# Kernel optimization log

Measured on AMD Instinct MI355X. Metric: run time of the kernel, lower is better.

## Reference

```python
import jax, jax.numpy as jnp
import numpy as np

N = 50000      # nodes
E = 400000     # edges (avg degree 8)
C = 128        # dim_single (node_dim)
DP = 64        # dim_pair (edge_dim)
HID = 256      # dim_egnn_hidden
DEPTH = 4      # depth_equivariant
M_IN = 2 * C + DP  # node_mlp / coord_mlp input dim = 320


def setup_inputs() -> dict:
    key = jax.random.key(0)
    ks = jax.random.split(key, 12)
    def w(k, shape, fan):
        return jax.random.normal(k, shape, jnp.float32) / np.float32(np.sqrt(fan))
    return {
        'single': jax.random.normal(ks[0], (N, C), jnp.float32),
        'pair': jax.random.normal(ks[1], (1,), jnp.float32),  # unused (se3t/ipa disabled)
        'coords': jax.random.normal(ks[2], (N, 3), jnp.float32),
        'edge_index': jax.random.randint(ks[3], (2, E), 0, N, jnp.int32),
        'edge_dist': jax.random.uniform(ks[4], (E,), jnp.float32),
        # stacked per-layer EGNN params (leading DEPTH axis, consumed by lax.scan)
        'We1': w(ks[5], (DEPTH, 1, DP), 1), 'be1': jnp.zeros((DEPTH, DP), jnp.float32),
        'We2': w(ks[6], (DEPTH, DP, DP), DP), 'be2': jnp.zeros((DEPTH, DP), jnp.float32),
        'Wn1': w(ks[7], (DEPTH, M_IN, HID), M_IN), 'bn1': jnp.zeros((DEPTH, HID), jnp.float32),
        'Wn2': w(ks[8], (DEPTH, HID, C), HID), 'bn2': jnp.zeros((DEPTH, C), jnp.float32),
        'Wc1': w(ks[9], (DEPTH, M_IN, HID), M_IN), 'bc1': jnp.zeros((DEPTH, HID), jnp.float32),
        'Wc2': w(ks[10], (DEPTH, HID, 1), HID),  # coord_mlp final layer has no bias
        'gamma': jnp.ones((C,), jnp.float32), 'beta': jnp.zeros((C,), jnp.float32),
    }


def _egnn_stack(h, x, edge_index, edge_dist, params):
    src, dst = edge_index[0], edge_index[1]
    n_nodes = h.shape[0]
    def layer(carry, p):
        h, x = carry
        We1, be1, We2, be2, Wn1, bn1, Wn2, bn2, Wc1, bc1, Wc2 = p
        # edge_mlp(edge_dist)
        ea = jax.nn.silu(edge_dist[:, None] @ We1 + be1) @ We2 + be2        # [E, DP]
        # gather -> concat -> MLP (message)
        mi = jnp.concatenate([h[src], h[dst], ea], axis=-1)                 # [E, 2C+DP]
        m = jax.nn.silu(mi @ Wn1 + bn1) @ Wn2 + bn2                         # [E, C]
        h = h + jax.ops.segment_sum(m, dst, num_segments=n_nodes)          # index_add on dst
        # coordinate update
        cw = jax.nn.silu(mi @ Wc1 + bc1) @ Wc2                              # [E, 1]
        x = x + jax.ops.segment_sum(cw * (x[src] - x[dst]), dst, num_segments=n_nodes)
        return (h, x), None
    (h, x), _ = jax.lax.scan(layer, (h, x), params)
    return h, x


def reference(single, pair, coords, edge_index, edge_dist,
              We1, be1, We2, be2, Wn1, bn1, Wn2, bn2, Wc1, bc1, Wc2,
              gamma, beta):
    h, x = _egnn_stack(single, coords, edge_index, edge_dist,
                       (We1, be1, We2, be2, Wn1, bn1, Wn2, bn2, Wc1, bc1, Wc2))
    # final LayerNorm (eps=1e-5, matching nn.LayerNorm default)
    mu = h.mean(-1, keepdims=True)
    var = ((h - mu) ** 2).mean(-1, keepdims=True)
    out = gamma * (h - mu) * jax.lax.rsqrt(var + 1e-5) + beta
    return out, x
```

## Files before the change

### kernel.cpp

```cpp
#include <hip/hip_runtime.h>
#include <hip/hip_bf16.h>
#include <math.h>

#define NN 50000
#define NE 400000
#define CD 128
#define EPB 64
#define HBINS 50176

typedef __attribute__((ext_vector_type(8))) short bf16x8;
typedef __attribute__((ext_vector_type(4))) float f32x4;

__device__ __forceinline__ float silu_f(float z) {
    return z * __builtin_amdgcn_rcpf(1.f + __expf(-z));
}
__device__ __forceinline__ unsigned short f2bf(float x) {
    unsigned int u = __float_as_uint(x);
    u = (u + 0x7FFFu + ((u >> 16) & 1u)) >> 16;
    return (unsigned short)u;
}
__device__ __forceinline__ float bf2f(unsigned short h) {
    return __uint_as_float(((unsigned int)h) << 16);
}
__device__ __forceinline__ unsigned pk_bf16(float a, float b) {
    union { __hip_bfloat162 h2; unsigned u; } cv;
    cv.h2 = __float22bfloat162_rn(make_float2(a, b));
    return cv.u;
}

__global__ __launch_bounds__(256) void hist_kernel(
        const int* __restrict__ dst, int* __restrict__ hist)
{
    int e = blockIdx.x * 256 + threadIdx.x;
    if (e < NE) atomicAdd(&hist[dst[e]], 1);
}

__global__ __launch_bounds__(256) void scan1_kernel(
        const int* __restrict__ hist, int* __restrict__ offs, int* __restrict__ bsum)
{
    __shared__ int sh[256];
    const int t = threadIdx.x;
    const int i = blockIdx.x * 256 + t;
    int v = hist[i];
    sh[t] = v;
    __syncthreads();
    for (int off = 1; off < 256; off <<= 1) {
        int x = (t >= off) ? sh[t - off] : 0;
        __syncthreads();
        sh[t] += x;
        __syncthreads();
    }
    offs[i] = sh[t] - v;
    if (t == 255) bsum[blockIdx.x] = sh[t];
}

__global__ __launch_bounds__(256) void scan2_kernel(int* __restrict__ bsum)
{
    __shared__ int sh[256];
    const int t = threadIdx.x;
    int v = (t < 196) ? bsum[t] : 0;
    sh[t] = v;
    __syncthreads();
    for (int off = 1; off < 256; off <<= 1) {
        int x = (t >= off) ? sh[t - off] : 0;
        __syncthreads();
        sh[t] += x;
        __syncthreads();
    }
    if (t < 196) bsum[t] = sh[t] - v;
}

__global__ __launch_bounds__(256) void scan3_kernel(
        const int* __restrict__ offs, const int* __restrict__ bsum,
        int* __restrict__ cursor)
{
    const int i = blockIdx.x * 256 + threadIdx.x;
    cursor[i] = offs[i] + bsum[blockIdx.x];
}

__global__ __launch_bounds__(256) void scatter_kernel(
        const int* __restrict__ eidx, const float* __restrict__ edist,
        int* __restrict__ cursor,
        int* __restrict__ ssrc, int* __restrict__ sdst, float* __restrict__ sdist)
{
    int e = blockIdx.x * 256 + threadIdx.x;
    if (e < NE) {
        int d = eidx[NE + e];
        int p = atomicAdd(&cursor[d], 1);
        ssrc[p] = eidx[e];
        sdst[p] = d;
        sdist[p] = edist[e];
    }
}

__global__ __launch_bounds__(64) void wbig_prep(
        const float* __restrict__ We2, const float* __restrict__ Wn1,
        const float* __restrict__ Wc1, unsigned short* __restrict__ wbig)
{
    const int l = blockIdx.y;
    const int ntile = blockIdx.x / 10;
    const int ks = blockIdx.x % 10;
    const int lane = threadIdx.x;
    const int n = ntile * 16 + (lane & 15);
    const int kbase = ks * 32 + (lane >> 4) * 8;
    const float* Wn1l = Wn1 + (size_t)l * 320 * 256;
    const float* Wc1l = Wc1 + (size_t)l * 320 * 256;
    const float* We2l = We2 + (size_t)l * 64 * 64;
    const float* W1 = (n < 256) ? Wn1l : Wc1l;
    const int nn = n & 255;
    unsigned short* outp = wbig + ((((size_t)l * 32 + ntile) * 10 + ks) * 64 + lane) * 8;
    #pragma unroll
    for (int j = 0; j < 8; ++j) {
        int k = kbase + j;
        float val;
        if (k < 256) {
            val = W1[(size_t)k * 256 + nn];
        } else {
            int i = k - 256;
            float acc = 0.f;
            #pragma unroll 8
            for (int jj = 0; jj < 64; ++jj)
                acc += We2l[i * 64 + jj] * W1[(size_t)(256 + jj) * 256 + nn];
            val = acc;
        }
        outp[j] = f2bf(val);
    }
}

__global__ __launch_bounds__(64) void wn2_prep(
        const float* __restrict__ Wn2, unsigned short* __restrict__ wn2s)
{
    const int l = blockIdx.y;
    const int ntile = blockIdx.x / 8;
    const int ks = blockIdx.x % 8;
    const int lane = threadIdx.x;
    const int n = ntile * 16 + (lane & 15);
    const int kbase = ks * 32 + (lane >> 4) * 8;
    const float* Wn2l = Wn2 + (size_t)l * 256 * 128;
    unsigned short* outp = wn2s + ((((size_t)l * 8 + ntile) * 8 + ks) * 64 + lane) * 8;
    #pragma unroll
    for (int j = 0; j < 8; ++j)
        outp[j] = f2bf(Wn2l[(size_t)(kbase + j) * 128 + n]);
}

__global__ __launch_bounds__(512) void cep_prep(
        const float* __restrict__ be2,
        const float* __restrict__ Wn1, const float* __restrict__ Wc1,
        const float* __restrict__ bn1, const float* __restrict__ bc1,
        float* __restrict__ cep)
{
    const int l = blockIdx.x;
    const int j = threadIdx.x;
    const int jj = j & 255;
    const float* W1 = ((j < 256) ? Wn1 : Wc1) + (size_t)l * 320 * 256;
    const float* be2l = be2 + l * 64;
    float acc = (j < 256) ? bn1[l * 256 + jj] : bc1[l * 256 + jj];
    #pragma unroll 8
    for (int k = 0; k < 64; ++k)
        acc += be2l[k] * W1[(size_t)(256 + k) * 256 + jj];
    cep[l * 512 + j] = acc;
}

__global__ __launch_bounds__(256) void conv_kernel(
        const float* __restrict__ h, unsigned short* __restrict__ hbf)
{
    const int i = (blockIdx.x * 256 + threadIdx.x) * 4;
    float4 v = *(const float4*)(h + i);
    *(uint2*)(hbf + i) = make_uint2(pk_bf16(v.x, v.y), pk_bf16(v.z, v.w));
}

__global__ __launch_bounds__(512, 4) void edge_kernel(
        const int* __restrict__ ssrc, const int* __restrict__ sdst,
        const float* __restrict__ sdist,
        const float* __restrict__ We1l, const float* __restrict__ be1l,
        const unsigned short* __restrict__ hbf,
        const unsigned short* __restrict__ wbig_l,
        const float* __restrict__ cep_l,
        const float* __restrict__ Wc2l,
        const float* __restrict__ x_in,
        float* __restrict__ Tbar, float* __restrict__ x_out)
{
    __shared__ __align__(16) unsigned short s_A[EPB][328];
    __shared__ __align__(16) unsigned short s_tT[256][72];
    __shared__ __align__(16) float s_cw[EPB][4];
    __shared__ __align__(16) unsigned short s_rid[EPB];
    __shared__ int s_src[EPB], s_dst[EPB];
    __shared__ int s_rdst[EPB];
    __shared__ unsigned long long s_mask;

    const int tid = threadIdx.x;
    const int eb = blockIdx.x * EPB;

    if (tid < EPB) {
        int dv = sdst[eb + tid];
        s_src[tid] = ssrc[eb + tid];
        s_dst[tid] = dv;
        int nxt = (tid == EPB - 1) ? -1 : sdst[eb + tid + 1];
        unsigned long long mk = __ballot(dv != nxt);
        int rid = __popcll(mk & ((1ull << tid) - 1ull));
        s_rid[tid] = (unsigned short)rid;
        if (dv != nxt) s_rdst[rid] = dv;
        if (tid == 0) s_mask = mk;
    }
    {
        const int e = tid >> 3;
        const int j0 = (tid & 7) * 8;
        const float d = sdist[eb + e];
        unsigned tmp[4];
        #pragma unroll
        for (int j = 0; j < 4; ++j) {
            float a = silu_f(d * We1l[j0 + 2 * j] + be1l[j0 + 2 * j]);
            float b = silu_f(d * We1l[j0 + 2 * j + 1] + be1l[j0 + 2 * j + 1]);
            tmp[j] = pk_bf16(a, b);
        }
        *(bf16x8*)&s_A[e][j0 + 256] = *(const bf16x8*)tmp;
    }
    __syncthreads();

    #pragma unroll
    for (int it = 0; it < 4; ++it) {
        const int c = tid + it * 512;
        const int row = c >> 5, ch = c & 31;
        const int node = (ch < 16) ? s_src[row] : s_dst[row];
        const int koff = (ch & 15) * 8;
        bf16x8 v = *(const bf16x8*)(hbf + (size_t)node * CD + koff);
        *(bf16x8*)&s_A[row][ch * 8] = v;
    }
    __syncthreads();

    const int wave = tid >> 6, lane = tid & 63;
    const int m = lane & 15, q = lane >> 4;

    f32x4 acc[4][4];
    #pragma unroll
    for (int nt = 0; nt < 4; ++nt)
        #pragma unroll
        for (int mt = 0; mt < 4; ++mt)
            acc[nt][mt] = (f32x4){0.f, 0.f, 0.f, 0.f};

    if (wave < 4) {
        #pragma unroll
        for (int ks = 0; ks < 10; ++ks) {
            const int koff = ks * 32 + q * 8;
            bf16x8 ef[4];
            #pragma unroll
            for (int mt = 0; mt < 4; ++mt)
                ef[mt] = *(const bf16x8*)&s_A[mt * 16 + m][koff];
            #pragma unroll
            for (int nt = 0; nt < 4; ++nt) {
                bf16x8 wf = *(const bf16x8*)(wbig_l +
                    ((size_t)((wave * 4 + nt) * 10 + ks) * 64 + lane) * 8);
                #pragma unroll
                for (int mt = 0; mt < 4; ++mt)
                    acc[nt][mt] = __builtin_amdgcn_mfma_f32_16x16x32_bf16(
                        ef[mt], wf, acc[nt][mt], 0, 0, 0);
            }
        }
    } else {
        #pragma unroll
        for (int ks = 0; ks < 10; ++ks) {
            const int koff = ks * 32 + q * 8;
            bf16x8 ef[4];
            #pragma unroll
            for (int mt = 0; mt < 4; ++mt)
                ef[mt] = *(const bf16x8*)&s_A[mt * 16 + m][koff];
            #pragma unroll
            for (int nt = 0; nt < 4; ++nt) {
                bf16x8 wf = *(const bf16x8*)(wbig_l +
                    ((size_t)((wave * 4 + nt) * 10 + ks) * 64 + lane) * 8);
                #pragma unroll
                for (int mt = 0; mt < 4; ++mt)
                    acc[nt][mt] = __builtin_amdgcn_mfma_f32_16x16x32_bf16(
                        wf, ef[mt], acc[nt][mt], 0, 0, 0);
            }
        }
    }

    if (wave < 4) {
        #pragma unroll
        for (int nt = 0; nt < 4; ++nt) {
            const int col = (wave * 4 + nt) * 16 + m;
            const float ce = cep_l[col];
            #pragma unroll
            for (int mt = 0; mt < 4; ++mt) {
                float t0 = silu_f(acc[nt][mt][0] + ce);
                float t1 = silu_f(acc[nt][mt][1] + ce);
                float t2 = silu_f(acc[nt][mt][2] + ce);
                float t3 = silu_f(acc[nt][mt][3] + ce);
                *(uint2*)&s_tT[col][(mt * 16 + q * 4) ^ ((m & 3) << 3)] =
                    make_uint2(pk_bf16(t0, t1), pk_bf16(t2, t3));
            }
        }
    } else {
        float p[4] = {0.f, 0.f, 0.f, 0.f};
        #pragma unroll
        for (int nt = 0; nt < 4; ++nt) {
            const int c0 = (wave * 4 + nt) * 16 + q * 4;
            const float4 ce = *(const float4*)&cep_l[c0];
            const float4 wv = *(const float4*)&Wc2l[c0 - 256];
            #pragma unroll
            for (int mt = 0; mt < 4; ++mt) {
                p[mt] += silu_f(acc[nt][mt][0] + ce.x) * wv.x;
                p[mt] += silu_f(acc[nt][mt][1] + ce.y) * wv.y;
                p[mt] += silu_f(acc[nt][mt][2] + ce.z) * wv.z;
                p[mt] += silu_f(acc[nt][mt][3] + ce.w) * wv.w;
            }
        }
        #pragma unroll
        for (int mt = 0; mt < 4; ++mt) {
            p[mt] += __shfl_xor(p[mt], 16);
            p[mt] += __shfl_xor(p[mt], 32);
        }
        if (lane < 16) {
            #pragma unroll
            for (int mt = 0; mt < 4; ++mt)
                s_cw[mt * 16 + lane][wave - 4] = p[mt];
        }
    }
    __syncthreads();

    {
        const unsigned long long mask = s_mask;
        const int nruns = __popcll(mask);
        f32x4 a2[2][4];
        #pragma unroll
        for (int mt2 = 0; mt2 < 2; ++mt2)
            #pragma unroll
            for (int nt = 0; nt < 4; ++nt)
                a2[mt2][nt] = (f32x4){0.f, 0.f, 0.f, 0.f};
        #pragma unroll
        for (int ks = 0; ks < 2; ++ks) {
            bf16x8 af[2];
            #pragma unroll
            for (int mt2 = 0; mt2 < 2; ++mt2)
                af[mt2] = *(const bf16x8*)&s_tT[(wave * 2 + mt2) * 16 + m]
                                           [(ks * 32 + q * 8) ^ ((m & 3) << 3)];
            const unsigned* rp = (const unsigned*)&s_rid[ks * 32 + q * 8];
            const unsigned r01 = rp[0], r23 = rp[1], r45 = rp[2], r67 = rp[3];
            #pragma unroll
            for (int nt = 0; nt < 4; ++nt) {
                const unsigned n = (unsigned)(nt * 16 + m);
                unsigned gw[4];
                gw[0] = ((r01 & 0xFFFFu) == n ? 0x3F80u : 0u) |
                        ((r01 >> 16)      == n ? 0x3F800000u : 0u);
                gw[1] = ((r23 & 0xFFFFu) == n ? 0x3F80u : 0u) |
                        ((r23 >> 16)      == n ? 0x3F800000u : 0u);
                gw[2] = ((r45 & 0xFFFFu) == n ? 0x3F80u : 0u) |
                        ((r45 >> 16)      == n ? 0x3F800000u : 0u);
                gw[3] = ((r67 & 0xFFFFu) == n ? 0x3F80u : 0u) |
                        ((r67 >> 16)      == n ? 0x3F800000u : 0u);
                const bf16x8 bfr = *(const bf16x8*)gw;
                #pragma unroll
                for (int mt2 = 0; mt2 < 2; ++mt2)
                    a2[mt2][nt] = __builtin_amdgcn_mfma_f32_16x16x32_bf16(
                        af[mt2], bfr, a2[mt2][nt], 0, 0, 0);
            }
        }
        #pragma unroll
        for (int nt = 0; nt < 4; ++nt) {
            const int r = nt * 16 + m;
            if (r < nruns) {
                float* bp = Tbar + (size_t)s_rdst[r] * 256;
                const bool bdry = (r == 0) || (r == nruns - 1);
                #pragma unroll
                for (int mt2 = 0; mt2 < 2; ++mt2) {
                    const int c = (wave * 2 + mt2) * 16 + q * 4;
                    if (bdry) {
                        atomicAdd(&bp[c],     a2[mt2][nt][0]);
                        atomicAdd(&bp[c + 1], a2[mt2][nt][1]);
                        atomicAdd(&bp[c + 2], a2[mt2][nt][2]);
                        atomicAdd(&bp[c + 3], a2[mt2][nt][3]);
                    } else {
                        *(f32x4*)&bp[c] = a2[mt2][nt];
                    }
                }
            }
        }
    }
    if (wave == 2) {
        const int e = lane;
        float4 pv = *(const float4*)&s_cw[e][0];
        float cw = pv.x + pv.y + pv.z + pv.w;
        int sn = s_src[e], dn = s_dst[e];
        float dx0 = x_in[sn * 3 + 0] - x_in[dn * 3 + 0];
        float dx1 = x_in[sn * 3 + 1] - x_in[dn * 3 + 1];
        float dx2 = x_in[sn * 3 + 2] - x_in[dn * 3 + 2];
        atomicAdd(&x_out[dn * 3 + 0], cw * dx0);
        atomicAdd(&x_out[dn * 3 + 1], cw * dx1);
        atomicAdd(&x_out[dn * 3 + 2], cw * dx2);
    }
}

__global__ __launch_bounds__(256) void node_kernel(
        const float* __restrict__ Tbar, const int* __restrict__ deg,
        const unsigned short* __restrict__ wn2_l, const float* __restrict__ bn2l,
        float* __restrict__ h, unsigned short* __restrict__ hbf)
{
    const int nb = blockIdx.x * 64;
    const int tid = threadIdx.x;
    const int wave = tid >> 6, lane = tid & 63;
    const int m = lane & 15, q = lane >> 4;

    f32x4 acc[2][4];
    #pragma unroll
    for (int nt = 0; nt < 2; ++nt)
        #pragma unroll
        for (int mt = 0; mt < 4; ++mt)
            acc[nt][mt] = (f32x4){0.f, 0.f, 0.f, 0.f};

    #pragma unroll
    for (int ks = 0; ks < 8; ++ks) {
        bf16x8 af[4];
        #pragma unroll
        for (int mt = 0; mt < 4; ++mt) {
            const int node = nb + mt * 16 + m;
            if (node < NN) {
                const float* tp = Tbar + (size_t)node * 256 + ks * 32 + q * 8;
                float4 f0 = *(const float4*)tp;
                float4 f1 = *(const float4*)(tp + 4);
                unsigned u[4] = { pk_bf16(f0.x, f0.y), pk_bf16(f0.z, f0.w),
                                  pk_bf16(f1.x, f1.y), pk_bf16(f1.z, f1.w) };
                af[mt] = *(const bf16x8*)u;
            } else {
                af[mt] = (bf16x8){0,0,0,0,0,0,0,0};
            }
        }
        #pragma unroll
        for (int nt = 0; nt < 2; ++nt) {
            bf16x8 wf = *(const bf16x8*)(wn2_l +
                ((size_t)((wave * 2 + nt) * 8 + ks) * 64 + lane) * 8);
            #pragma unroll
            for (int mt = 0; mt < 4; ++mt)
                acc[nt][mt] = __builtin_amdgcn_mfma_f32_16x16x32_bf16(af[mt], wf, acc[nt][mt], 0, 0, 0);
        }
    }
    #pragma unroll
    for (int nt = 0; nt < 2; ++nt) {
        const int col = (wave * 2 + nt) * 16 + m;
        const float bb = bn2l[col];
        #pragma unroll
        for (int mt = 0; mt < 4; ++mt) {
            #pragma unroll
            for (int i = 0; i < 4; ++i) {
                const int node = nb + mt * 16 + q * 4 + i;
                if (node < NN) {
                    float val = acc[nt][mt][i] + (float)deg[node] * bb
                              + h[(size_t)node * CD + col];
                    h[(size_t)node * CD + col] = val;
                    hbf[(size_t)node * CD + col] = f2bf(val);
                }
            }
        }
    }
}

__global__ __launch_bounds__(256) void final_kernel(
        const float* __restrict__ h, const float* __restrict__ x,
        const float* __restrict__ gamma, const float* __restrict__ beta,
        float* __restrict__ out)
{
    const int lane = threadIdx.x & 63;
    const int wave = threadIdx.x >> 6;
    const int n = blockIdx.x * 4 + wave;
    float v0 = h[(size_t)n * CD + lane];
    float v1 = h[(size_t)n * CD + 64 + lane];
    float ssum = v0 + v1;
    for (int off = 32; off; off >>= 1) ssum += __shfl_xor(ssum, off);
    float mu = ssum * (1.f / 128.f);
    float d0 = v0 - mu, d1 = v1 - mu;
    float sq = d0 * d0 + d1 * d1;
    for (int off = 32; off; off >>= 1) sq += __shfl_xor(sq, off);
    float rstd = rsqrtf(sq * (1.f / 128.f) + 1e-5f);
    out[(size_t)n * CD + lane]      = gamma[lane]      * d0 * rstd + beta[lane];
    out[(size_t)n * CD + 64 + lane] = gamma[64 + lane] * d1 * rstd + beta[64 + lane];
    if (threadIdx.x < 12) {
        int nn = blockIdx.x * 4 + threadIdx.x / 3;
        int c = threadIdx.x % 3;
        out[(size_t)NN * CD + nn * 3 + c] = x[nn * 3 + c];
    }
}

static inline size_t align_up(size_t v) { return (v + 255) & ~(size_t)255; }

extern "C" void kernel_launch(void* const* d_in, const int* in_sizes, int n_in,
                              void* d_out, int out_size, void* d_ws, size_t ws_size,
                              hipStream_t stream)
{
    const float* single = (const float*)d_in[0];
    const float* coords = (const float*)d_in[2];
    const int*   eidx   = (const int*)d_in[3];
    const float* edist  = (const float*)d_in[4];
    const float* We1 = (const float*)d_in[5];
    const float* be1 = (const float*)d_in[6];
    const float* We2 = (const float*)d_in[7];
    const float* be2 = (const float*)d_in[8];
    const float* Wn1 = (const float*)d_in[9];
    const float* bn1 = (const float*)d_in[10];
    const float* Wn2 = (const float*)d_in[11];
    const float* bn2 = (const float*)d_in[12];
    const float* Wc1 = (const float*)d_in[13];
    const float* bc1 = (const float*)d_in[14];
    const float* Wc2 = (const float*)d_in[15];
    const float* gamma = (const float*)d_in[16];
    const float* beta  = (const float*)d_in[17];
    float* out = (float*)d_out;

    char* w = (char*)d_ws;
    float* h0  = (float*)w;  w += align_up((size_t)NN * CD * 4);
    float* x0  = (float*)w;  w += align_up((size_t)NN * 3 * 4);
    float* x1  = (float*)w;  w += align_up((size_t)NN * 3 * 4);
    unsigned short* hbf  = (unsigned short*)w; w += align_up((size_t)NN * CD * 2);
    unsigned short* wbig = (unsigned short*)w; w += align_up((size_t)4 * 512 * 320 * 2);
    unsigned short* wn2s = (unsigned short*)w; w += align_up((size_t)4 * 256 * 128 * 2);
    float* cep = (float*)w;  w += align_up((size_t)4 * 512 * 4);
    int* hist   = (int*)w;   w += align_up((size_t)HBINS * 4);
    int* offs   = (int*)w;   w += align_up((size_t)HBINS * 4);
    int* cursor = (int*)w;   w += align_up((size_t)HBINS * 4);
    int* bsum   = (int*)w;   w += align_up((size_t)256 * 4);
    int* ssrc   = (int*)w;   w += align_up((size_t)NE * 4);
    int* sdst   = (int*)w;   w += align_up((size_t)NE * 4);
    float* sdist = (float*)w; w += align_up((size_t)NE * 4);
    float* Tbar = (float*)w; w += align_up((size_t)NN * 256 * 4);

    hipMemsetAsync(hist, 0, (size_t)HBINS * 4, stream);
    hist_kernel<<<(NE + 255) / 256, 256, 0, stream>>>(eidx + NE, hist);
    scan1_kernel<<<HBINS / 256, 256, 0, stream>>>(hist, offs, bsum);
    scan2_kernel<<<1, 256, 0, stream>>>(bsum);
    scan3_kernel<<<HBINS / 256, 256, 0, stream>>>(offs, bsum, cursor);
    scatter_kernel<<<(NE + 255) / 256, 256, 0, stream>>>(eidx, edist, cursor, ssrc, sdst, sdist);

    wbig_prep<<<dim3(320, 4), 64, 0, stream>>>(We2, Wn1, Wc1, wbig);
    wn2_prep<<<dim3(64, 4), 64, 0, stream>>>(Wn2, wn2s);
    cep_prep<<<4, 512, 0, stream>>>(be2, Wn1, Wc1, bn1, bc1, cep);

    hipMemcpyAsync(h0, single, (size_t)NN * CD * 4, hipMemcpyDeviceToDevice, stream);
    hipMemcpyAsync(x0, coords, (size_t)NN * 3 * 4, hipMemcpyDeviceToDevice, stream);
    conv_kernel<<<(NN * CD) / 1024, 256, 0, stream>>>(single, hbf);

    float* xc = x0; float* xn = x1;
    for (int l = 0; l < 4; ++l) {
        hipMemsetAsync(Tbar, 0, (size_t)NN * 256 * 4, stream);
        hipMemcpyAsync(xn, xc, (size_t)NN * 3 * 4, hipMemcpyDeviceToDevice, stream);
        edge_kernel<<<NE / EPB, 512, 0, stream>>>(
            ssrc, sdst, sdist,
            We1 + l * 64, be1 + l * 64,
            hbf,
            wbig + (size_t)l * 512 * 320,
            cep + l * 512,
            Wc2 + l * 256,
            xc, Tbar, xn);
        node_kernel<<<(NN + 63) / 64, 256, 0, stream>>>(
            Tbar, hist,
            wn2s + (size_t)l * 256 * 128,
            bn2 + l * CD, h0, hbf);
        float* t = xc; xc = xn; xn = t;
    }
    final_kernel<<<NN / 4, 256, 0, stream>>>(h0, xc, gamma, beta, out);
}
```

Measured before the change: 1.362 ms.

## Replace full Tbar memset with boundary zeroing and use direct-to-LDS gathers

```diff
diff --git a/kernel.cpp b/kernel.cpp
--- a/kernel.cpp
+++ b/kernel.cpp
@@ -19,13 +19,15 @@
     u = (u + 0x7FFFu + ((u >> 16) & 1u)) >> 16;
     return (unsigned short)u;
 }
-__device__ __forceinline__ float bf2f(unsigned short h) {
-    return __uint_as_float(((unsigned int)h) << 16);
-}
 __device__ __forceinline__ unsigned pk_bf16(float a, float b) {
     union { __hip_bfloat162 h2; unsigned u; } cv;
     cv.h2 = __float22bfloat162_rn(make_float2(a, b));
     return cv.u;
+}
+__device__ __forceinline__ void gload_lds16(const unsigned short* g, unsigned short* l) {
+    __builtin_amdgcn_global_load_lds(
+        (const __attribute__((address_space(1))) unsigned int*)g,
+        (__attribute__((address_space(3))) unsigned int*)l, 16, 0, 0);
 }
 
 __global__ __launch_bounds__(256) void hist_kernel(
@@ -169,6 +171,16 @@
     *(uint2*)(hbf + i) = make_uint2(pk_bf16(v.x, v.y), pk_bf16(v.z, v.w));
 }
 
+__global__ __launch_bounds__(128) void zbdry_kernel(
+        const int* __restrict__ sdst, float* __restrict__ Tbar)
+{
+    const int b = blockIdx.x;
+    const int t = threadIdx.x;
+    const int r = (t < 64) ? sdst[b * EPB] : sdst[b * EPB + EPB - 1];
+    *(float4*)(Tbar + (size_t)r * 256 + (t & 63) * 4) =
+        make_float4(0.f, 0.f, 0.f, 0.f);
+}
+
 __global__ __launch_bounds__(512, 4) void edge_kernel(
         const int* __restrict__ ssrc, const int* __restrict__ sdst,
         const float* __restrict__ sdist,
@@ -180,7 +192,8 @@
         const float* __restrict__ x_in,
         float* __restrict__ Tbar, float* __restrict__ x_out)
 {
-    __shared__ __align__(16) unsigned short s_A[EPB][328];
+    __shared__ __align__(16) unsigned short s_h[EPB][256];
+    __shared__ __align__(16) unsigned short s_e[EPB][72];
     __shared__ __align__(16) unsigned short s_tT[256][72];
     __shared__ __align__(16) float s_cw[EPB][4];
     __shared__ __align__(16) unsigned short s_rid[EPB];
@@ -213,18 +226,18 @@
             float b = silu_f(d * We1l[j0 + 2 * j + 1] + be1l[j0 + 2 * j + 1]);
             tmp[j] = pk_bf16(a, b);
         }
-        *(bf16x8*)&s_A[e][j0 + 256] = *(const bf16x8*)tmp;
+        *(bf16x8*)&s_e[e][j0] = *(const bf16x8*)tmp;
     }
     __syncthreads();
 
     #pragma unroll
     for (int it = 0; it < 4; ++it) {
-        const int c = tid + it * 512;
-        const int row = c >> 5, ch = c & 31;
-        const int node = (ch < 16) ? s_src[row] : s_dst[row];
-        const int koff = (ch & 15) * 8;
-        bf16x8 v = *(const bf16x8*)(hbf + (size_t)node * CD + koff);
-        *(bf16x8*)&s_A[row][ch * 8] = v;
+        const int slot = tid + it * 512;
+        const int row = slot >> 5;
+        const int c = (slot & 31) ^ (row & 7);
+        const int node = (c < 16) ? s_src[row] : s_dst[row];
+        gload_lds16(hbf + (size_t)node * CD + (c & 15) * 8,
+                    &s_h[0][0] + slot * 8);
     }
     __syncthreads();
 
@@ -241,11 +254,14 @@
     if (wave < 4) {
         #pragma unroll
         for (int ks = 0; ks < 10; ++ks) {
-            const int koff = ks * 32 + q * 8;
             bf16x8 ef[4];
             #pragma unroll
-            for (int mt = 0; mt < 4; ++mt)
-                ef[mt] = *(const bf16x8*)&s_A[mt * 16 + m][koff];
+            for (int mt = 0; mt < 4; ++mt) {
+                const int row = mt * 16 + m;
+                ef[mt] = (ks < 8)
+                    ? *(const bf16x8*)&s_h[row][((ks * 4 + q) ^ (m & 7)) * 8]
+                    : *(const bf16x8*)&s_e[row][(ks - 8) * 32 + q * 8];
+            }
             #pragma unroll
             for (int nt = 0; nt < 4; ++nt) {
                 bf16x8 wf = *(const bf16x8*)(wbig_l +
@@ -259,11 +275,14 @@
     } else {
         #pragma unroll
         for (int ks = 0; ks < 10; ++ks) {
-            const int koff = ks * 32 + q * 8;
             bf16x8 ef[4];
             #pragma unroll
-            for (int mt = 0; mt < 4; ++mt)
-                ef[mt] = *(const bf16x8*)&s_A[mt * 16 + m][koff];
+            for (int mt = 0; mt < 4; ++mt) {
+                const int row = mt * 16 + m;
+                ef[mt] = (ks < 8)
+                    ? *(const bf16x8*)&s_h[row][((ks * 4 + q) ^ (m & 7)) * 8]
+                    : *(const bf16x8*)&s_e[row][(ks - 8) * 32 + q * 8];
+            }
             #pragma unroll
             for (int nt = 0; nt < 4; ++nt) {
                 bf16x8 wf = *(const bf16x8*)(wbig_l +
@@ -401,6 +420,13 @@
     const int wave = tid >> 6, lane = tid & 63;
     const int m = lane & 15, q = lane >> 4;
 
+    int dg[4];
+    #pragma unroll
+    for (int mt = 0; mt < 4; ++mt) {
+        const int node = nb + mt * 16 + m;
+        dg[mt] = (node < NN) ? deg[node] : 0;
+    }
+
     f32x4 acc[2][4];
     #pragma unroll
     for (int nt = 0; nt < 2; ++nt)
@@ -414,7 +440,7 @@
         #pragma unroll
         for (int mt = 0; mt < 4; ++mt) {
             const int node = nb + mt * 16 + m;
-            if (node < NN) {
+            if (dg[mt] != 0) {
                 const float* tp = Tbar + (size_t)node * 256 + ks * 32 + q * 8;
                 float4 f0 = *(const float4*)tp;
                 float4 f1 = *(const float4*)(tp + 4);
@@ -539,7 +565,7 @@
 
     float* xc = x0; float* xn = x1;
     for (int l = 0; l < 4; ++l) {
-        hipMemsetAsync(Tbar, 0, (size_t)NN * 256 * 4, stream);
+        zbdry_kernel<<<NE / EPB, 128, 0, stream>>>(sdst, Tbar);
         hipMemcpyAsync(xn, xc, (size_t)NN * 3 * 4, hipMemcpyDeviceToDevice, stream);
         edge_kernel<<<NE / EPB, 512, 0, stream>>>(
             ssrc, sdst, sdist,
```

Result: slower. 1.520 ms (+11.6%).
